# Kernel optimization log

Measured on AMD Instinct MI355X. Metric: run time of the kernel, lower is better.

The kernel has to match this reference:

```python
import jax, jax.numpy as jnp
import numpy as np

KERNEL_MUL = 2.0
KERNEL_NUM = 5


def _mmd(source, target):
    n_s = source.shape[0]
    total = jnp.concatenate([source, target], axis=0)  # (2N, D)
    n = total.shape[0]
    # pairwise squared L2 via a^2 + b^2 - 2ab (avoids (2N,2N,D) intermediate)
    sq = jnp.sum(total * total, axis=1)  # (2N,)
    L2 = sq[:, None] + sq[None, :] - 2.0 * (total @ total.T)  # (2N, 2N)
    # torch uses L2_distance.data for bandwidth -> stop_gradient
    bandwidth = jax.lax.stop_gradient(jnp.sum(L2)) / (n * n - n)
    bandwidth = bandwidth / (KERNEL_MUL ** (KERNEL_NUM // 2))
    # multi-bandwidth RBF sum
    kernels = jnp.zeros_like(L2)
    for i in range(KERNEL_NUM):
        kernels = kernels + jnp.exp(-L2 / (bandwidth * KERNEL_MUL ** i))
    XX = kernels[:n_s, :n_s]
    YY = kernels[n_s:, n_s:]
    XY = kernels[:n_s, n_s:]
    YX = kernels[n_s:, :n_s]
    return jnp.mean(XX) + jnp.mean(YY) - jnp.mean(XY) - jnp.mean(YX)


def setup_inputs() -> dict:
    key = jax.random.key(0)
    k1, k2 = jax.random.split(key)
    source = jax.random.normal(k1, (4096, 256), dtype=jnp.float32)
    target = jax.random.normal(k2, (4096, 256), dtype=jnp.float32) + 0.5
    return {"source": source, "target": target}


def reference(source, target):
    return _mmd(source, target)
```

## Files before the change

### kernel.cpp

```cpp
#include <hip/hip_runtime.h>

typedef short bf16x8 __attribute__((ext_vector_type(8)));
typedef float f32x4 __attribute__((ext_vector_type(4)));

#define KDIM 256
#define BT 128
#define BK 64

__device__ __forceinline__ unsigned short f2bf(float f) {
  unsigned u = __float_as_uint(f);
  unsigned r = (u + 0x7fffu + ((u >> 16) & 1u)) >> 16;
  return (unsigned short)r;
}
__device__ __forceinline__ float bf2f(unsigned short b) {
  return __uint_as_float(((unsigned)b) << 16);
}

__device__ __forceinline__ void async_cp16(const void* g, void* l) {
  __builtin_amdgcn_global_load_lds(
      (const __attribute__((address_space(1))) unsigned int*)g,
      (__attribute__((address_space(3))) unsigned int*)l, 16, 0, 0);
}

__global__ __launch_bounds__(256) void mmd_stage(
    const float* __restrict__ src, const float* __restrict__ tgt, int ns,
    unsigned short* __restrict__ Tbf, float* __restrict__ sq,
    float* __restrict__ scol, float* __restrict__ sum_sq) {
  __shared__ float sp[256];
  __shared__ float rw[4];
  int t = threadIdx.x;
  int lane = t & 63, wave = t >> 6;
  sp[t] = 0.f;
  __syncthreads();
  int sub = t & 31;
  int rsel = t >> 5;
  float colacc[8];
#pragma unroll
  for (int j = 0; j < 8; ++j) colacc[j] = 0.f;
  float tsq = 0.f;
#pragma unroll
  for (int it = 0; it < 4; ++it) {
    int r = blockIdx.x * 32 + it * 8 + rsel;
    const float* rp = (r < ns) ? (src + (size_t)r * KDIM)
                               : (tgt + (size_t)(r - ns) * KDIM);
    float4 v0 = *(const float4*)(rp + sub * 8);
    float4 v1 = *(const float4*)(rp + sub * 8 + 4);
    float vals[8] = {v0.x, v0.y, v0.z, v0.w, v1.x, v1.y, v1.z, v1.w};
    unsigned pk[4];
    float ssp = 0.f;
#pragma unroll
    for (int j = 0; j < 4; ++j) {
      unsigned short b0 = f2bf(vals[2 * j]);
      unsigned short b1 = f2bf(vals[2 * j + 1]);
      float x0 = bf2f(b0), x1 = bf2f(b1);
      pk[j] = (unsigned)b0 | ((unsigned)b1 << 16);
      ssp += x0 * x0 + x1 * x1;
      colacc[2 * j] += x0;
      colacc[2 * j + 1] += x1;
    }
    *(uint4*)(Tbf + (size_t)r * KDIM + sub * 8) =
        make_uint4(pk[0], pk[1], pk[2], pk[3]);
    tsq += ssp;
    float ss = ssp;
#pragma unroll
    for (int off = 16; off; off >>= 1) ss += __shfl_down(ss, off, 32);
    if (sub == 0) sq[r] = ss;
  }
#pragma unroll
  for (int j = 0; j < 8; ++j) atomicAdd(&sp[sub * 8 + j], colacc[j]);
#pragma unroll
  for (int off = 32; off; off >>= 1) tsq += __shfl_down(tsq, off, 64);
  if (lane == 0) rw[wave] = tsq;
  __syncthreads();
  atomicAdd(&scol[t], sp[t]);
  if (t == 0) atomicAdd(sum_sq, rw[0] + rw[1] + rw[2] + rw[3]);
}

__global__ void mmd_prep2(const float* __restrict__ scol,
                          const float* __restrict__ sum_sq,
                          float* __restrict__ coef, float* __restrict__ out,
                          int n) {
  int t = threadIdx.x;
  float4 v = *(const float4*)(scol + t * 4);
  float p = v.x * v.x + v.y * v.y + v.z * v.z + v.w * v.w;
#pragma unroll
  for (int off = 32; off; off >>= 1) p += __shfl_down(p, off, 64);
  if (t == 0) {
    double ssq = (double)p;
    double S = (double)sum_sq[0];
    double nn = (double)n;
    double sumL2 = 2.0 * nn * S - 2.0 * ssq;
    double bw = sumL2 / (nn * nn - nn) / 4.0;
    double l2e = 1.4426950408889634;
#pragma unroll
    for (int i = 0; i < 5; ++i)
      coef[i] = (float)(-l2e / (bw * (double)(1 << i)));
    out[0] = 0.f;
  }
}

__device__ __forceinline__ float2 pk_add(float2 a, float2 b) {
  return make_float2(a.x + b.x, a.y + b.y);
}
__device__ __forceinline__ float2 pk_mul(float2 a, float2 b) {
  return make_float2(a.x * b.x, a.y * b.y);
}
__device__ __forceinline__ float2 pk_fma(float2 a, float2 b, float2 c) {
  return make_float2(__builtin_fmaf(a.x, b.x, c.x),
                     __builtin_fmaf(a.y, b.y, c.y));
}

__global__ __launch_bounds__(256) void mmd_main(
    const unsigned short* __restrict__ Tbf, const float* __restrict__ sq,
    const float* __restrict__ coef, float* __restrict__ out, int halfTiles,
    float inv) {
  __shared__ short As[BT * BK];
  __shared__ short Bs[BT * BK];
  __shared__ float sqa[BT];
  __shared__ float sqb[BT];
  __shared__ float red[4];

  int id = blockIdx.x;
  int bi = (int)((sqrtf(8.f * (float)id + 1.f) - 1.f) * 0.5f);
  while ((bi + 1) * (bi + 2) / 2 <= id) ++bi;
  while (bi * (bi + 1) / 2 > id) --bi;
  int bj = id - bi * (bi + 1) / 2;
  int rowBase = bi * BT, colBase = bj * BT;

  int t = threadIdx.x;
  int lane = t & 63, wave = t >> 6;

  if (t < 128) sqa[t] = sq[rowBase + t];
  else sqb[t - 128] = sq[colBase + (t - 128)];

  f32x4 acc[4][4];
#pragma unroll
  for (int a = 0; a < 4; ++a)
#pragma unroll
    for (int b = 0; b < 4; ++b) {
      f32x4 z = {0.f, 0.f, 0.f, 0.f};
      acc[a][b] = z;
    }

  int wrow = (wave >> 1) * 64, wcol = (wave & 1) * 64;
  int lrow = lane >> 3;
  int kgsw = (lane & 7) ^ lrow;
  int frow = lane & 15;
  int kq = lane >> 4;

  for (int c = 0; c < 4; ++c) {
    int k0 = c * BK;
#pragma unroll
    for (int j = 0; j < 4; ++j) {
      int R0 = j * 32 + wave * 8;
      int ldsoff = (j * 256 + wave * 64) * 8;
      async_cp16(Tbf + (size_t)(rowBase + R0 + lrow) * KDIM + k0 + kgsw * 8,
                 &As[ldsoff]);
      async_cp16(Tbf + (size_t)(colBase + R0 + lrow) * KDIM + k0 + kgsw * 8,
                 &Bs[ldsoff]);
    }
    __syncthreads();
#pragma unroll
    for (int ks = 0; ks < 2; ++ks) {
      bf16x8 af[4], bfv[4];
#pragma unroll
      for (int mt = 0; mt < 4; ++mt) {
        int r = wrow + mt * 16 + frow;
        int pg = (ks * 4 + kq) ^ (r & 7);
        af[mt] = *(const bf16x8*)&As[r * BK + pg * 8];
      }
#pragma unroll
      for (int nt = 0; nt < 4; ++nt) {
        int r = wcol + nt * 16 + frow;
        int pg = (ks * 4 + kq) ^ (r & 7);
        bfv[nt] = *(const bf16x8*)&Bs[r * BK + pg * 8];
      }
#pragma unroll
      for (int mt = 0; mt < 4; ++mt)
#pragma unroll
        for (int nt = 0; nt < 4; ++nt)
          acc[mt][nt] = __builtin_amdgcn_mfma_f32_16x16x32_bf16(
              af[mt], bfv[nt], acc[mt][nt], 0, 0, 0);
    }
    __syncthreads();
  }

  float c4 = coef[4];
  float m2c4 = -2.f * c4;
  float2 m2v = make_float2(m2c4, m2c4);
  int ccol = lane & 15;
  int rb = (lane >> 4) * 4;
  float ra[16];
#pragma unroll
  for (int mt = 0; mt < 4; ++mt)
#pragma unroll
    for (int rg = 0; rg < 4; ++rg)
      ra[mt * 4 + rg] = sqa[wrow + mt * 16 + rb + rg] * c4;
  float cbv[4];
#pragma unroll
  for (int nt = 0; nt < 4; ++nt) cbv[nt] = sqb[wcol + nt * 16 + ccol] * c4;

  float2 lsum2 = make_float2(0.f, 0.f);
#pragma unroll
  for (int mt = 0; mt < 4; ++mt) {
#pragma unroll
    for (int nt = 0; nt < 4; ++nt) {
      float cb = cbv[nt];
#pragma unroll
      for (int rp = 0; rp < 4; rp += 2) {
        float2 g = make_float2(acc[mt][nt][rp], acc[mt][nt][rp + 1]);
        float2 sab = make_float2(ra[mt * 4 + rp] + cb, ra[mt * 4 + rp + 1] + cb);
        float2 u = pk_fma(g, m2v, sab);
        float2 e = make_float2(__builtin_amdgcn_exp2f(u.x),
                               __builtin_amdgcn_exp2f(u.y));
        float2 e2 = pk_mul(e, e);
        float2 e4 = pk_mul(e2, e2);
        float2 e8 = pk_mul(e4, e4);
        float2 s = pk_add(e, e2);
        s = pk_add(s, e4);
        s = pk_add(s, e8);
        s = pk_fma(e8, e8, s);
        lsum2 = pk_add(lsum2, s);
      }
    }
  }
  float lsum = lsum2.x + lsum2.y;
#pragma unroll
  for (int off = 32; off; off >>= 1) lsum += __shfl_down(lsum, off, 64);
  if (lane == 0) red[wave] = lsum;
  __syncthreads();
  if (t == 0) {
    float w = ((bi < halfTiles) == (bj < halfTiles)) ? 1.f : -1.f;
    float f = (bi == bj) ? 1.f : 2.f;
    atomicAdd(out, w * f * inv * (red[0] + red[1] + red[2] + red[3]));
  }
}

extern "C" void kernel_launch(void* const* d_in, const int* in_sizes, int n_in,
                              void* d_out, int out_size, void* d_ws,
                              size_t ws_size, hipStream_t stream) {
  const float* src = (const float*)d_in[0];
  const float* tgt = (const float*)d_in[1];
  int ns = in_sizes[0] / KDIM;
  int ntr = in_sizes[1] / KDIM;
  int n = ns + ntr;

  char* ws = (char*)d_ws;
  unsigned short* Tbf = (unsigned short*)ws;
  size_t off = (size_t)n * KDIM * sizeof(unsigned short);
  float* sq = (float*)(ws + off);     off += (size_t)n * 4;
  float* scol = (float*)(ws + off);   off += (size_t)KDIM * 4;
  float* sum_sq = (float*)(ws + off); off += 4;
  float* coef = (float*)(ws + off);

  hipMemsetAsync(scol, 0, (KDIM + 1) * sizeof(float), stream);

  mmd_stage<<<n / 32, 256, 0, stream>>>(src, tgt, ns, Tbf, sq, scol, sum_sq);
  mmd_prep2<<<1, 64, 0, stream>>>(scol, sum_sq, coef, (float*)d_out, n);
  int nb = n / BT;
  int nblk = nb * (nb + 1) / 2;
  mmd_main<<<nblk, 256, 0, stream>>>(Tbf, sq, coef, (float*)d_out, ns / BT,
                                     1.f / ((float)ns * (float)ns));
}
```

Baseline: 113.1 us.

## Use 256x256 tiles with double-buffered async loads and fold prep into main

Grows the output tile from 128x128 with 4 waves to 256x256 with 8 waves and double-buffers the K-chunk loads into dynamic LDS, controlled by explicit vmcnt waits, barriers and setprio around the MFMA phases. A fixed grid of 512 blocks handles the triangular tile set, with the first blocks taking a second tile. The separate single-block prep kernel is removed: its bandwidth computation moves into each main block and output zeroing moves into the stage kernel. This is meant to raise data reuse, hide global load latency and drop one launch, at the cost of 128KB of LDS per block, heavy register pressure from 32 accumulators and uneven work across blocks.

```diff
diff --git a/kernel.cpp b/kernel.cpp
--- a/kernel.cpp
+++ b/kernel.cpp
@@ -4,8 +4,8 @@
 typedef float f32x4 __attribute__((ext_vector_type(4)));
 
 #define KDIM 256
-#define BT 128
-#define BK 64
+#define BT 256
+#define TILE_SH (256 * 64)
 
 __device__ __forceinline__ unsigned short f2bf(float f) {
   unsigned u = __float_as_uint(f);
@@ -25,10 +25,12 @@
 __global__ __launch_bounds__(256) void mmd_stage(
     const float* __restrict__ src, const float* __restrict__ tgt, int ns,
     unsigned short* __restrict__ Tbf, float* __restrict__ sq,
-    float* __restrict__ scol, float* __restrict__ sum_sq) {
+    float* __restrict__ scol, float* __restrict__ sum_sq,
+    float* __restrict__ out) {
   __shared__ float sp[256];
   __shared__ float rw[4];
   int t = threadIdx.x;
+  if (blockIdx.x == 0 && t == 0) out[0] = 0.f;
   int lane = t & 63, wave = t >> 6;
   sp[t] = 0.f;
   __syncthreads();
@@ -76,29 +78,6 @@
   if (t == 0) atomicAdd(sum_sq, rw[0] + rw[1] + rw[2] + rw[3]);
 }
 
-__global__ void mmd_prep2(const float* __restrict__ scol,
-                          const float* __restrict__ sum_sq,
-                          float* __restrict__ coef, float* __restrict__ out,
-                          int n) {
-  int t = threadIdx.x;
-  float4 v = *(const float4*)(scol + t * 4);
-  float p = v.x * v.x + v.y * v.y + v.z * v.z + v.w * v.w;
-#pragma unroll
-  for (int off = 32; off; off >>= 1) p += __shfl_down(p, off, 64);
-  if (t == 0) {
-    double ssq = (double)p;
-    double S = (double)sum_sq[0];
-    double nn = (double)n;
-    double sumL2 = 2.0 * nn * S - 2.0 * ssq;
-    double bw = sumL2 / (nn * nn - nn) / 4.0;
-    double l2e = 1.4426950408889634;
-#pragma unroll
-    for (int i = 0; i < 5; ++i)
-      coef[i] = (float)(-l2e / (bw * (double)(1 << i)));
-    out[0] = 0.f;
-  }
-}
-
 __device__ __forceinline__ float2 pk_add(float2 a, float2 b) {
   return make_float2(a.x + b.x, a.y + b.y);
 }
@@ -110,129 +89,226 @@
                      __builtin_fmaf(a.y, b.y, c.y));
 }
 
-__global__ __launch_bounds__(256) void mmd_main(
+#define BAR() __builtin_amdgcn_s_barrier()
+#define LGKM0() asm volatile("s_waitcnt lgkmcnt(0)" ::: "memory")
+#define VMC8() asm volatile("s_waitcnt vmcnt(8)" ::: "memory")
+#define VMC0() asm volatile("s_waitcnt vmcnt(0)" ::: "memory")
+
+__global__ __launch_bounds__(512, 2) void mmd_main(
     const unsigned short* __restrict__ Tbf, const float* __restrict__ sq,
-    const float* __restrict__ coef, float* __restrict__ out, int halfTiles,
-    float inv) {
-  __shared__ short As[BT * BK];
-  __shared__ short Bs[BT * BK];
-  __shared__ float sqa[BT];
-  __shared__ float sqb[BT];
-  __shared__ float red[4];
-
-  int id = blockIdx.x;
-  int bi = (int)((sqrtf(8.f * (float)id + 1.f) - 1.f) * 0.5f);
-  while ((bi + 1) * (bi + 2) / 2 <= id) ++bi;
-  while (bi * (bi + 1) / 2 > id) --bi;
-  int bj = id - bi * (bi + 1) / 2;
-  int rowBase = bi * BT, colBase = bj * BT;
+    const float* __restrict__ scol, const float* __restrict__ sum_sq,
+    float* __restrict__ out, int n, int halfTiles, int extra, float inv) {
+  extern __shared__ __align__(16) short smem[];
+  short* As = smem;
+  short* Bs = smem + 2 * TILE_SH;
+  __shared__ float s_c4;
+  __shared__ float red[8];
 
   int t = threadIdx.x;
-  int lane = t & 63, wave = t >> 6;
-
-  if (t < 128) sqa[t] = sq[rowBase + t];
-  else sqb[t - 128] = sq[colBase + (t - 128)];
-
-  f32x4 acc[4][4];
-#pragma unroll
-  for (int a = 0; a < 4; ++a)
-#pragma unroll
-    for (int b = 0; b < 4; ++b) {
-      f32x4 z = {0.f, 0.f, 0.f, 0.f};
-      acc[a][b] = z;
-    }
-
-  int wrow = (wave >> 1) * 64, wcol = (wave & 1) * 64;
-  int lrow = lane >> 3;
-  int kgsw = (lane & 7) ^ lrow;
+  int lane = t & 63, w = t >> 6;
+
+  if (w == 0) {
+    float4 v = *(const float4*)(scol + lane * 4);
+    float p = v.x * v.x + v.y * v.y + v.z * v.z + v.w * v.w;
+#pragma unroll
+    for (int off = 32; off; off >>= 1) p += __shfl_down(p, off, 64);
+    if (lane == 0) {
+      double ssq = (double)p, S = (double)sum_sq[0], nn = (double)n;
+      double bwv = (2.0 * nn * S - 2.0 * ssq) / (nn * nn - nn) / 4.0;
+      s_c4 = (float)(-1.4426950408889634 / (bwv * 16.0));
+    }
+  }
+
+  int trow = t >> 3;
+  int kg = (t & 7) ^ (trow & 7);
+  int ldsb = w * 8 * 64;
+
+  int wrow = (w >> 2) * 128;
+  int wcol = (w & 3) * 64;
   int frow = lane & 15;
   int kq = lane >> 4;
-
-  for (int c = 0; c < 4; ++c) {
-    int k0 = c * BK;
-#pragma unroll
-    for (int j = 0; j < 4; ++j) {
-      int R0 = j * 32 + wave * 8;
-      int ldsoff = (j * 256 + wave * 64) * 8;
-      async_cp16(Tbf + (size_t)(rowBase + R0 + lrow) * KDIM + k0 + kgsw * 8,
-                 &As[ldsoff]);
-      async_cp16(Tbf + (size_t)(colBase + R0 + lrow) * KDIM + k0 + kgsw * 8,
-                 &Bs[ldsoff]);
-    }
-    __syncthreads();
-#pragma unroll
-    for (int ks = 0; ks < 2; ++ks) {
-      bf16x8 af[4], bfv[4];
-#pragma unroll
-      for (int mt = 0; mt < 4; ++mt) {
-        int r = wrow + mt * 16 + frow;
-        int pg = (ks * 4 + kq) ^ (r & 7);
-        af[mt] = *(const bf16x8*)&As[r * BK + pg * 8];
+  int colk0 = (kq ^ (frow & 7)) * 8;
+  int aoff[4], boff[4];
+#pragma unroll
+  for (int mt = 0; mt < 4; ++mt) aoff[mt] = (wrow + mt * 16 + frow) * 64;
+#pragma unroll
+  for (int nt = 0; nt < 4; ++nt) boff[nt] = (wcol + nt * 16 + frow) * 64;
+
+  int b = blockIdx.x;
+  int nrep = (b < extra) ? 2 : 1;
+  int id0 = (b < extra) ? b : b + extra;
+
+  for (int rep = 0; rep < nrep; ++rep) {
+    int id = id0 + rep * extra;
+    int bi = (int)((sqrtf(8.f * (float)id + 1.f) - 1.f) * 0.5f);
+    while ((bi + 1) * (bi + 2) / 2 <= id) ++bi;
+    while (bi * (bi + 1) / 2 > id) --bi;
+    int bj = id - bi * (bi + 1) / 2;
+    int rowBase = bi * BT, colBase = bj * BT;
+
+    const unsigned short* ga = Tbf + (size_t)(rowBase + trow) * KDIM + kg * 8;
+    const unsigned short* gb = Tbf + (size_t)(colBase + trow) * KDIM + kg * 8;
+
+    auto stage = [&](int tt) {
+      short* Ad = As + (tt & 1) * TILE_SH;
+      short* Bd = Bs + (tt & 1) * TILE_SH;
+      const unsigned short* gA = ga + tt * 64;
+      const unsigned short* gB = gb + tt * 64;
+#pragma unroll
+      for (int j = 0; j < 4; ++j) {
+        async_cp16(gA + (size_t)j * 64 * KDIM, &Ad[j * 64 * 64 + ldsb]);
+        async_cp16(gB + (size_t)j * 64 * KDIM, &Bd[j * 64 * 64 + ldsb]);
       }
-#pragma unroll
-      for (int nt = 0; nt < 4; ++nt) {
-        int r = wcol + nt * 16 + frow;
-        int pg = (ks * 4 + kq) ^ (r & 7);
-        bfv[nt] = *(const bf16x8*)&Bs[r * BK + pg * 8];
+    };
+
+    f32x4 acc[8][4];
+#pragma unroll
+    for (int a = 0; a < 8; ++a)
+#pragma unroll
+      for (int c = 0; c < 4; ++c) {
+        f32x4 z = {0.f, 0.f, 0.f, 0.f};
+        acc[a][c] = z;
       }
+
+    stage(0);
+    stage(1);
+
+#pragma unroll
+    for (int tt = 0; tt < 4; ++tt) {
+      if (tt >= 1 && tt <= 2) stage(tt + 1);
+      if (tt < 3) VMC8();
+      else VMC0();
+      BAR();
+
+      const short* Ab = As + (tt & 1) * TILE_SH;
+      const short* Bb = Bs + (tt & 1) * TILE_SH;
+      bf16x8 aL[4], aH[4], bv[4];
+
+#pragma unroll
+      for (int mt = 0; mt < 4; ++mt)
+        aL[mt] = *(const bf16x8*)&Ab[aoff[mt] + colk0];
+#pragma unroll
+      for (int nt = 0; nt < 4; ++nt)
+        bv[nt] = *(const bf16x8*)&Bb[boff[nt] + colk0];
+      BAR();
+      LGKM0();
+      __builtin_amdgcn_s_setprio(1);
 #pragma unroll
       for (int mt = 0; mt < 4; ++mt)
 #pragma unroll
         for (int nt = 0; nt < 4; ++nt)
           acc[mt][nt] = __builtin_amdgcn_mfma_f32_16x16x32_bf16(
-              af[mt], bfv[nt], acc[mt][nt], 0, 0, 0);
-    }
+              aL[mt], bv[nt], acc[mt][nt], 0, 0, 0);
+      __builtin_amdgcn_s_setprio(0);
+      BAR();
+
+#pragma unroll
+      for (int mt = 0; mt < 4; ++mt)
+        aH[mt] = *(const bf16x8*)&Ab[aoff[mt] + 4096 + colk0];
+      BAR();
+      LGKM0();
+      __builtin_amdgcn_s_setprio(1);
+#pragma unroll
+      for (int mt = 0; mt < 4; ++mt)
+#pragma unroll
+        for (int nt = 0; nt < 4; ++nt)
+          acc[4 + mt][nt] = __builtin_amdgcn_mfma_f32_16x16x32_bf16(
+              aH[mt], bv[nt], acc[4 + mt][nt], 0, 0, 0);
+      __builtin_amdgcn_s_setprio(0);
+      BAR();
+
+#pragma unroll
+      for (int mt = 0; mt < 4; ++mt)
+        aL[mt] = *(const bf16x8*)&Ab[aoff[mt] + (colk0 ^ 32)];
+#pragma unroll
+      for (int nt = 0; nt < 4; ++nt)
+        bv[nt] = *(const bf16x8*)&Bb[boff[nt] + (colk0 ^ 32)];
+      BAR();
+      LGKM0();
+      __builtin_amdgcn_s_setprio(1);
+#pragma unroll
+      for (int mt = 0; mt < 4; ++mt)
+#pragma unroll
+        for (int nt = 0; nt < 4; ++nt)
+          acc[mt][nt] = __builtin_amdgcn_mfma_f32_16x16x32_bf16(
+              aL[mt], bv[nt], acc[mt][nt], 0, 0, 0);
+      __builtin_amdgcn_s_setprio(0);
+      BAR();
+
+#pragma unroll
+      for (int mt = 0; mt < 4; ++mt)
+        aH[mt] = *(const bf16x8*)&Ab[aoff[mt] + 4096 + (colk0 ^ 32)];
+      BAR();
+      LGKM0();
+      __builtin_amdgcn_s_setprio(1);
+#pragma unroll
+      for (int mt = 0; mt < 4; ++mt)
+#pragma unroll
+        for (int nt = 0; nt < 4; ++nt)
+          acc[4 + mt][nt] = __builtin_amdgcn_mfma_f32_16x16x32_bf16(
+              aH[mt], bv[nt], acc[4 + mt][nt], 0, 0, 0);
+      __builtin_amdgcn_s_setprio(0);
+      BAR();
+    }
+
+    float c4 = s_c4;
+    float m2c4 = -2.f * c4;
+    float2 m2v = make_float2(m2c4, m2c4);
+    int ccol = lane & 15;
+    int rb = (lane >> 4) * 4;
+    const float* sqa = sq + rowBase;
+    const float* sqb = sq + colBase;
+    float ra[32];
+#pragma unroll
+    for (int mt = 0; mt < 8; ++mt) {
+      float4 rv = *(const float4*)(sqa + wrow + mt * 16 + rb);
+      ra[mt * 4 + 0] = rv.x * c4;
+      ra[mt * 4 + 1] = rv.y * c4;
+      ra[mt * 4 + 2] = rv.z * c4;
+      ra[mt * 4 + 3] = rv.w * c4;
+    }
+    float cbv[4];
+#pragma unroll
+    for (int nt = 0; nt < 4; ++nt) cbv[nt] = sqb[wcol + nt * 16 + ccol] * c4;
+
+    float2 lsum2 = make_float2(0.f, 0.f);
+#pragma unroll
+    for (int mt = 0; mt < 8; ++mt) {
+#pragma unroll
+      for (int nt = 0; nt < 4; ++nt) {
+        float cb = cbv[nt];
+#pragma unroll
+        for (int rp = 0; rp < 4; rp += 2) {
+          float2 g = make_float2(acc[mt][nt][rp], acc[mt][nt][rp + 1]);
+          float2 sab =
+              make_float2(ra[mt * 4 + rp] + cb, ra[mt * 4 + rp + 1] + cb);
+          float2 u = pk_fma(g, m2v, sab);
+          float2 e = make_float2(__builtin_amdgcn_exp2f(u.x),
+                                 __builtin_amdgcn_exp2f(u.y));
+          float2 e2 = pk_mul(e, e);
+          float2 e4 = pk_mul(e2, e2);
+          float2 e8 = pk_mul(e4, e4);
+          float2 s = pk_add(e, e2);
+          s = pk_add(s, e4);
+          s = pk_add(s, e8);
+          s = pk_fma(e8, e8, s);
+          lsum2 = pk_add(lsum2, s);
+        }
+      }
+    }
+    float lsum = lsum2.x + lsum2.y;
+#pragma unroll
+    for (int off = 32; off; off >>= 1) lsum += __shfl_down(lsum, off, 64);
+    if (lane == 0) red[w] = lsum;
     __syncthreads();
-  }
-
-  float c4 = coef[4];
-  float m2c4 = -2.f * c4;
-  float2 m2v = make_float2(m2c4, m2c4);
-  int ccol = lane & 15;
-  int rb = (lane >> 4) * 4;
-  float ra[16];
-#pragma unroll
-  for (int mt = 0; mt < 4; ++mt)
-#pragma unroll
-    for (int rg = 0; rg < 4; ++rg)
-      ra[mt * 4 + rg] = sqa[wrow + mt * 16 + rb + rg] * c4;
-  float cbv[4];
-#pragma unroll
-  for (int nt = 0; nt < 4; ++nt) cbv[nt] = sqb[wcol + nt * 16 + ccol] * c4;
-
-  float2 lsum2 = make_float2(0.f, 0.f);
-#pragma unroll
-  for (int mt = 0; mt < 4; ++mt) {
-#pragma unroll
-    for (int nt = 0; nt < 4; ++nt) {
-      float cb = cbv[nt];
-#pragma unroll
-      for (int rp = 0; rp < 4; rp += 2) {
-        float2 g = make_float2(acc[mt][nt][rp], acc[mt][nt][rp + 1]);
-        float2 sab = make_float2(ra[mt * 4 + rp] + cb, ra[mt * 4 + rp + 1] + cb);
-        float2 u = pk_fma(g, m2v, sab);
-        float2 e = make_float2(__builtin_amdgcn_exp2f(u.x),
-                               __builtin_amdgcn_exp2f(u.y));
-        float2 e2 = pk_mul(e, e);
-        float2 e4 = pk_mul(e2, e2);
-        float2 e8 = pk_mul(e4, e4);
-        float2 s = pk_add(e, e2);
-        s = pk_add(s, e4);
-        s = pk_add(s, e8);
-        s = pk_fma(e8, e8, s);
-        lsum2 = pk_add(lsum2, s);
-      }
-    }
-  }
-  float lsum = lsum2.x + lsum2.y;
-#pragma unroll
-  for (int off = 32; off; off >>= 1) lsum += __shfl_down(lsum, off, 64);
-  if (lane == 0) red[wave] = lsum;
-  __syncthreads();
-  if (t == 0) {
-    float w = ((bi < halfTiles) == (bj < halfTiles)) ? 1.f : -1.f;
-    float f = (bi == bj) ? 1.f : 2.f;
-    atomicAdd(out, w * f * inv * (red[0] + red[1] + red[2] + red[3]));
+    if (t == 0) {
+      float wsign = ((bi < halfTiles) == (bj < halfTiles)) ? 1.f : -1.f;
+      float f = (bi == bj) ? 1.f : 2.f;
+      float s = red[0] + red[1] + red[2] + red[3] + red[4] + red[5] + red[6] +
+                red[7];
+      atomicAdd(out, wsign * f * inv * s);
+    }
+    __syncthreads();
   }
 }
 
@@ -250,15 +326,22 @@
   size_t off = (size_t)n * KDIM * sizeof(unsigned short);
   float* sq = (float*)(ws + off);     off += (size_t)n * 4;
   float* scol = (float*)(ws + off);   off += (size_t)KDIM * 4;
-  float* sum_sq = (float*)(ws + off); off += 4;
-  float* coef = (float*)(ws + off);
+  float* sum_sq = (float*)(ws + off);
 
   hipMemsetAsync(scol, 0, (KDIM + 1) * sizeof(float), stream);
 
-  mmd_stage<<<n / 32, 256, 0, stream>>>(src, tgt, ns, Tbf, sq, scol, sum_sq);
-  mmd_prep2<<<1, 64, 0, stream>>>(scol, sum_sq, coef, (float*)d_out, n);
+  mmd_stage<<<n / 32, 256, 0, stream>>>(src, tgt, ns, Tbf, sq, scol, sum_sq,
+                                        (float*)d_out);
+
   int nb = n / BT;
-  int nblk = nb * (nb + 1) / 2;
-  mmd_main<<<nblk, 256, 0, stream>>>(Tbf, sq, coef, (float*)d_out, ns / BT,
-                                     1.f / ((float)ns * (float)ns));
-}
+  int ntiles = nb * (nb + 1) / 2;
+  int grid = 512;
+  int extra = ntiles - grid;
+  if (extra < 0) { grid = ntiles; extra = 0; }
+  int dyn = 4 * TILE_SH * (int)sizeof(short);
+  hipFuncSetAttribute(reinterpret_cast<const void*>(mmd_main),
+                      hipFuncAttributeMaxDynamicSharedMemorySize, dyn);
+  mmd_main<<<grid, 512, dyn, stream>>>(Tbf, sq, scol, sum_sq, (float*)d_out, n,
+                                       ns / BT, extra,
+                                       1.f / ((float)ns * (float)ns));
+}
```

Result: no change. 114.4 us (+1.2%).

## Fold bandwidth prep into main kernel and switch to 32x32x16 MFMA tiles

Applied to the files above, without the earlier changes.

Removes the single-block prep kernel launch: each main-kernel block now recomputes the bandwidth coefficient from the column sums, and the stage kernel zeroes the output. The GEMM inner loop switches from 16x16x32 to 32x32x16 bf16 MFMA with 2x2 accumulator tiles per wave, which means fewer LDS fragment loads per MFMA. The epilogue is reworked to match the new accumulator layout and reads the row norms as vector loads. This trades one launch plus a dependency gap for a small amount of redundant per-block reduction work.

```diff
diff --git a/kernel.cpp b/kernel.cpp
--- a/kernel.cpp
+++ b/kernel.cpp
@@ -2,6 +2,7 @@
 
 typedef short bf16x8 __attribute__((ext_vector_type(8)));
 typedef float f32x4 __attribute__((ext_vector_type(4)));
+typedef float f32x16 __attribute__((ext_vector_type(16)));
 
 #define KDIM 256
 #define BT 128
@@ -25,10 +26,12 @@
 __global__ __launch_bounds__(256) void mmd_stage(
     const float* __restrict__ src, const float* __restrict__ tgt, int ns,
     unsigned short* __restrict__ Tbf, float* __restrict__ sq,
-    float* __restrict__ scol, float* __restrict__ sum_sq) {
+    float* __restrict__ scol, float* __restrict__ sum_sq,
+    float* __restrict__ out) {
   __shared__ float sp[256];
   __shared__ float rw[4];
   int t = threadIdx.x;
+  if (blockIdx.x == 0 && t == 0) out[0] = 0.f;
   int lane = t & 63, wave = t >> 6;
   sp[t] = 0.f;
   __syncthreads();
@@ -76,29 +79,6 @@
   if (t == 0) atomicAdd(sum_sq, rw[0] + rw[1] + rw[2] + rw[3]);
 }
 
-__global__ void mmd_prep2(const float* __restrict__ scol,
-                          const float* __restrict__ sum_sq,
-                          float* __restrict__ coef, float* __restrict__ out,
-                          int n) {
-  int t = threadIdx.x;
-  float4 v = *(const float4*)(scol + t * 4);
-  float p = v.x * v.x + v.y * v.y + v.z * v.z + v.w * v.w;
-#pragma unroll
-  for (int off = 32; off; off >>= 1) p += __shfl_down(p, off, 64);
-  if (t == 0) {
-    double ssq = (double)p;
-    double S = (double)sum_sq[0];
-    double nn = (double)n;
-    double sumL2 = 2.0 * nn * S - 2.0 * ssq;
-    double bw = sumL2 / (nn * nn - nn) / 4.0;
-    double l2e = 1.4426950408889634;
-#pragma unroll
-    for (int i = 0; i < 5; ++i)
-      coef[i] = (float)(-l2e / (bw * (double)(1 << i)));
-    out[0] = 0.f;
-  }
-}
-
 __device__ __forceinline__ float2 pk_add(float2 a, float2 b) {
   return make_float2(a.x + b.x, a.y + b.y);
 }
@@ -112,13 +92,14 @@
 
 __global__ __launch_bounds__(256) void mmd_main(
     const unsigned short* __restrict__ Tbf, const float* __restrict__ sq,
-    const float* __restrict__ coef, float* __restrict__ out, int halfTiles,
-    float inv) {
+    const float* __restrict__ scol, const float* __restrict__ sum_sq,
+    float* __restrict__ out, int n, int halfTiles, float inv) {
   __shared__ short As[BT * BK];
   __shared__ short Bs[BT * BK];
   __shared__ float sqa[BT];
   __shared__ float sqb[BT];
   __shared__ float red[4];
+  __shared__ float s_c4;
 
   int id = blockIdx.x;
   int bi = (int)((sqrtf(8.f * (float)id + 1.f) - 1.f) * 0.5f);
@@ -130,23 +111,34 @@
   int t = threadIdx.x;
   int lane = t & 63, wave = t >> 6;
 
+  if (wave == 0) {
+    float4 v = *(const float4*)(scol + lane * 4);
+    float p = v.x * v.x + v.y * v.y + v.z * v.z + v.w * v.w;
+#pragma unroll
+    for (int off = 32; off; off >>= 1) p += __shfl_down(p, off, 64);
+    if (lane == 0) {
+      double ssq = (double)p, S = (double)sum_sq[0], nn = (double)n;
+      double bwv = (2.0 * nn * S - 2.0 * ssq) / (nn * nn - nn) / 4.0;
+      s_c4 = (float)(-1.4426950408889634 / (bwv * 16.0));
+    }
+  }
+
   if (t < 128) sqa[t] = sq[rowBase + t];
   else sqb[t - 128] = sq[colBase + (t - 128)];
 
-  f32x4 acc[4][4];
-#pragma unroll
-  for (int a = 0; a < 4; ++a)
-#pragma unroll
-    for (int b = 0; b < 4; ++b) {
-      f32x4 z = {0.f, 0.f, 0.f, 0.f};
-      acc[a][b] = z;
-    }
+  f32x16 acc[2][2];
+#pragma unroll
+  for (int a = 0; a < 2; ++a)
+#pragma unroll
+    for (int b = 0; b < 2; ++b)
+#pragma unroll
+      for (int e = 0; e < 16; ++e) acc[a][b][e] = 0.f;
 
   int wrow = (wave >> 1) * 64, wcol = (wave & 1) * 64;
   int lrow = lane >> 3;
   int kgsw = (lane & 7) ^ lrow;
-  int frow = lane & 15;
-  int kq = lane >> 4;
+  int frow = lane & 31;
+  int khalf = lane >> 5;
 
   for (int c = 0; c < 4; ++c) {
     int k0 = c * BK;
@@ -161,66 +153,64 @@
     }
     __syncthreads();
 #pragma unroll
-    for (int ks = 0; ks < 2; ++ks) {
-      bf16x8 af[4], bfv[4];
-#pragma unroll
-      for (int mt = 0; mt < 4; ++mt) {
-        int r = wrow + mt * 16 + frow;
-        int pg = (ks * 4 + kq) ^ (r & 7);
+    for (int ks = 0; ks < 4; ++ks) {
+      int o = ks * 2 + khalf;
+      bf16x8 af[2], bfv[2];
+#pragma unroll
+      for (int mt = 0; mt < 2; ++mt) {
+        int r = wrow + mt * 32 + frow;
+        int pg = o ^ (r & 7);
         af[mt] = *(const bf16x8*)&As[r * BK + pg * 8];
       }
 #pragma unroll
-      for (int nt = 0; nt < 4; ++nt) {
-        int r = wcol + nt * 16 + frow;
-        int pg = (ks * 4 + kq) ^ (r & 7);
+      for (int nt = 0; nt < 2; ++nt) {
+        int r = wcol + nt * 32 + frow;
+        int pg = o ^ (r & 7);
         bfv[nt] = *(const bf16x8*)&Bs[r * BK + pg * 8];
       }
 #pragma unroll
-      for (int mt = 0; mt < 4; ++mt)
-#pragma unroll
-        for (int nt = 0; nt < 4; ++nt)
-          acc[mt][nt] = __builtin_amdgcn_mfma_f32_16x16x32_bf16(
+      for (int mt = 0; mt < 2; ++mt)
+#pragma unroll
+        for (int nt = 0; nt < 2; ++nt)
+          acc[mt][nt] = __builtin_amdgcn_mfma_f32_32x32x16_bf16(
               af[mt], bfv[nt], acc[mt][nt], 0, 0, 0);
     }
     __syncthreads();
   }
 
-  float c4 = coef[4];
+  float c4 = s_c4;
   float m2c4 = -2.f * c4;
   float2 m2v = make_float2(m2c4, m2c4);
-  int ccol = lane & 15;
-  int rb = (lane >> 4) * 4;
-  float ra[16];
-#pragma unroll
-  for (int mt = 0; mt < 4; ++mt)
-#pragma unroll
-    for (int rg = 0; rg < 4; ++rg)
-      ra[mt * 4 + rg] = sqa[wrow + mt * 16 + rb + rg] * c4;
-  float cbv[4];
-#pragma unroll
-  for (int nt = 0; nt < 4; ++nt) cbv[nt] = sqb[wcol + nt * 16 + ccol] * c4;
-
+  int rb = khalf * 4;
   float2 lsum2 = make_float2(0.f, 0.f);
 #pragma unroll
-  for (int mt = 0; mt < 4; ++mt) {
-#pragma unroll
-    for (int nt = 0; nt < 4; ++nt) {
-      float cb = cbv[nt];
-#pragma unroll
-      for (int rp = 0; rp < 4; rp += 2) {
-        float2 g = make_float2(acc[mt][nt][rp], acc[mt][nt][rp + 1]);
-        float2 sab = make_float2(ra[mt * 4 + rp] + cb, ra[mt * 4 + rp + 1] + cb);
-        float2 u = pk_fma(g, m2v, sab);
-        float2 e = make_float2(__builtin_amdgcn_exp2f(u.x),
-                               __builtin_amdgcn_exp2f(u.y));
-        float2 e2 = pk_mul(e, e);
-        float2 e4 = pk_mul(e2, e2);
-        float2 e8 = pk_mul(e4, e4);
-        float2 s = pk_add(e, e2);
-        s = pk_add(s, e4);
-        s = pk_add(s, e8);
-        s = pk_fma(e8, e8, s);
-        lsum2 = pk_add(lsum2, s);
+  for (int mt = 0; mt < 2; ++mt) {
+    f32x4 rq[4];
+#pragma unroll
+    for (int q = 0; q < 4; ++q)
+      rq[q] = *(const f32x4*)&sqa[wrow + mt * 32 + 8 * q + rb];
+#pragma unroll
+    for (int nt = 0; nt < 2; ++nt) {
+      float cb = sqb[wcol + nt * 32 + frow] * c4;
+#pragma unroll
+      for (int q = 0; q < 4; ++q) {
+#pragma unroll
+        for (int s = 0; s < 4; s += 2) {
+          float2 g =
+              make_float2(acc[mt][nt][q * 4 + s], acc[mt][nt][q * 4 + s + 1]);
+          float2 sab = make_float2(rq[q][s] * c4 + cb, rq[q][s + 1] * c4 + cb);
+          float2 u = pk_fma(g, m2v, sab);
+          float2 e = make_float2(__builtin_amdgcn_exp2f(u.x),
+                                 __builtin_amdgcn_exp2f(u.y));
+          float2 e2 = pk_mul(e, e);
+          float2 e4 = pk_mul(e2, e2);
+          float2 e8 = pk_mul(e4, e4);
+          float2 sm = pk_add(e, e2);
+          sm = pk_add(sm, e4);
+          sm = pk_add(sm, e8);
+          sm = pk_fma(e8, e8, sm);
+          lsum2 = pk_add(lsum2, sm);
+        }
       }
     }
   }
@@ -250,15 +240,15 @@
   size_t off = (size_t)n * KDIM * sizeof(unsigned short);
   float* sq = (float*)(ws + off);     off += (size_t)n * 4;
   float* scol = (float*)(ws + off);   off += (size_t)KDIM * 4;
-  float* sum_sq = (float*)(ws + off); off += 4;
-  float* coef = (float*)(ws + off);
+  float* sum_sq = (float*)(ws + off);
 
   hipMemsetAsync(scol, 0, (KDIM + 1) * sizeof(float), stream);
 
-  mmd_stage<<<n / 32, 256, 0, stream>>>(src, tgt, ns, Tbf, sq, scol, sum_sq);
-  mmd_prep2<<<1, 64, 0, stream>>>(scol, sum_sq, coef, (float*)d_out, n);
+  mmd_stage<<<n / 32, 256, 0, stream>>>(src, tgt, ns, Tbf, sq, scol, sum_sq,
+                                        (float*)d_out);
+
   int nb = n / BT;
   int nblk = nb * (nb + 1) / 2;
-  mmd_main<<<nblk, 256, 0, stream>>>(Tbf, sq, coef, (float*)d_out, ns / BT,
-                                     1.f / ((float)ns * (float)ns));
-}
+  mmd_main<<<nblk, 256, 0, stream>>>(Tbf, sq, scol, sum_sq, (float*)d_out, n,
+                                     ns / BT, 1.f / ((float)ns * (float)ns));
+}
```

Result: slower. 118.3 us (+4.6%).

## Fold bandwidth prep into main kernel and replace atomic output with partial reduction

Applied to the files above, without the earlier changes.

Removes the single-block prep kernel by having every main block compute the bandwidth coefficient redundantly from the column sums and squared-norm total, which saves one launch and its dependency gap. Replaces the per-block atomicAdd to the output scalar with per-block partial writes followed by a small deterministic reduce kernel. That adds a launch back and a little redundant work per block, while removing atomic contention on the output and the separate output initialisation.

```diff
diff --git a/kernel.cpp b/kernel.cpp
--- a/kernel.cpp
+++ b/kernel.cpp
@@ -76,29 +76,6 @@
   if (t == 0) atomicAdd(sum_sq, rw[0] + rw[1] + rw[2] + rw[3]);
 }
 
-__global__ void mmd_prep2(const float* __restrict__ scol,
-                          const float* __restrict__ sum_sq,
-                          float* __restrict__ coef, float* __restrict__ out,
-                          int n) {
-  int t = threadIdx.x;
-  float4 v = *(const float4*)(scol + t * 4);
-  float p = v.x * v.x + v.y * v.y + v.z * v.z + v.w * v.w;
-#pragma unroll
-  for (int off = 32; off; off >>= 1) p += __shfl_down(p, off, 64);
-  if (t == 0) {
-    double ssq = (double)p;
-    double S = (double)sum_sq[0];
-    double nn = (double)n;
-    double sumL2 = 2.0 * nn * S - 2.0 * ssq;
-    double bw = sumL2 / (nn * nn - nn) / 4.0;
-    double l2e = 1.4426950408889634;
-#pragma unroll
-    for (int i = 0; i < 5; ++i)
-      coef[i] = (float)(-l2e / (bw * (double)(1 << i)));
-    out[0] = 0.f;
-  }
-}
-
 __device__ __forceinline__ float2 pk_add(float2 a, float2 b) {
   return make_float2(a.x + b.x, a.y + b.y);
 }
@@ -112,13 +89,14 @@
 
 __global__ __launch_bounds__(256) void mmd_main(
     const unsigned short* __restrict__ Tbf, const float* __restrict__ sq,
-    const float* __restrict__ coef, float* __restrict__ out, int halfTiles,
-    float inv) {
+    const float* __restrict__ scol, const float* __restrict__ sum_sq,
+    float* __restrict__ partials, int n, int halfTiles, float inv) {
   __shared__ short As[BT * BK];
   __shared__ short Bs[BT * BK];
   __shared__ float sqa[BT];
   __shared__ float sqb[BT];
   __shared__ float red[4];
+  __shared__ float s_c4;
 
   int id = blockIdx.x;
   int bi = (int)((sqrtf(8.f * (float)id + 1.f) - 1.f) * 0.5f);
@@ -129,6 +107,18 @@
 
   int t = threadIdx.x;
   int lane = t & 63, wave = t >> 6;
+
+  if (wave == 0) {
+    float4 v = *(const float4*)(scol + lane * 4);
+    float p = v.x * v.x + v.y * v.y + v.z * v.z + v.w * v.w;
+#pragma unroll
+    for (int off = 32; off; off >>= 1) p += __shfl_down(p, off, 64);
+    if (lane == 0) {
+      double ssq = (double)p, S = (double)sum_sq[0], nn = (double)n;
+      double bwv = (2.0 * nn * S - 2.0 * ssq) / (nn * nn - nn) / 4.0;
+      s_c4 = (float)(-1.4426950408889634 / (bwv * 16.0));
+    }
+  }
 
   if (t < 128) sqa[t] = sq[rowBase + t];
   else sqb[t - 128] = sq[colBase + (t - 128)];
@@ -185,7 +175,7 @@
     __syncthreads();
   }
 
-  float c4 = coef[4];
+  float c4 = s_c4;
   float m2c4 = -2.f * c4;
   float2 m2v = make_float2(m2c4, m2c4);
   int ccol = lane & 15;
@@ -232,8 +222,22 @@
   if (t == 0) {
     float w = ((bi < halfTiles) == (bj < halfTiles)) ? 1.f : -1.f;
     float f = (bi == bj) ? 1.f : 2.f;
-    atomicAdd(out, w * f * inv * (red[0] + red[1] + red[2] + red[3]));
-  }
+    partials[id] = w * f * inv * (red[0] + red[1] + red[2] + red[3]);
+  }
+}
+
+__global__ __launch_bounds__(256) void mmd_reduce(
+    const float* __restrict__ partials, int nblk, float* __restrict__ out) {
+  __shared__ float red[4];
+  int t = threadIdx.x;
+  int lane = t & 63, wave = t >> 6;
+  float a = 0.f;
+  for (int j = t; j < nblk; j += 256) a += partials[j];
+#pragma unroll
+  for (int off = 32; off; off >>= 1) a += __shfl_down(a, off, 64);
+  if (lane == 0) red[wave] = a;
+  __syncthreads();
+  if (t == 0) out[0] = red[0] + red[1] + red[2] + red[3];
 }
 
 extern "C" void kernel_launch(void* const* d_in, const int* in_sizes, int n_in,
@@ -248,17 +252,18 @@
   char* ws = (char*)d_ws;
   unsigned short* Tbf = (unsigned short*)ws;
   size_t off = (size_t)n * KDIM * sizeof(unsigned short);
-  float* sq = (float*)(ws + off);     off += (size_t)n * 4;
-  float* scol = (float*)(ws + off);   off += (size_t)KDIM * 4;
-  float* sum_sq = (float*)(ws + off); off += 4;
-  float* coef = (float*)(ws + off);
+  float* sq = (float*)(ws + off);       off += (size_t)n * 4;
+  float* scol = (float*)(ws + off);     off += (size_t)KDIM * 4;
+  float* sum_sq = (float*)(ws + off);   off += 4;
+  float* partials = (float*)(ws + off);
 
   hipMemsetAsync(scol, 0, (KDIM + 1) * sizeof(float), stream);
 
   mmd_stage<<<n / 32, 256, 0, stream>>>(src, tgt, ns, Tbf, sq, scol, sum_sq);
-  mmd_prep2<<<1, 64, 0, stream>>>(scol, sum_sq, coef, (float*)d_out, n);
+
   int nb = n / BT;
   int nblk = nb * (nb + 1) / 2;
-  mmd_main<<<nblk, 256, 0, stream>>>(Tbf, sq, coef, (float*)d_out, ns / BT,
-                                     1.f / ((float)ns * (float)ns));
-}
+  mmd_main<<<nblk, 256, 0, stream>>>(Tbf, sq, scol, sum_sq, partials, n,
+                                     ns / BT, 1.f / ((float)ns * (float)ns));
+  mmd_reduce<<<1, 256, 0, stream>>>(partials, nblk, (float*)d_out);
+}
```

After: 107.7 us. 4.8% less time.
